# Performance work log

Hardware: AMD Instinct MI355X
Metric: run time of the kernel (lower is better)

## Reference

```python
import jax, jax.numpy as jnp
import numpy as np

NEG_INF = -1e30  # finite stand-in for -inf (fp16/bf16-safe)


def _ctc_loss(log_probs, labels):
    """CTC negative log-likelihood per example (blank index = 0).

    log_probs: [T, B, V] log-softmaxed logits (time-major, as tf.nn.ctc_loss default)
    labels:    [B, L] int labels in [1, V)
    returns:   [B] per-example loss
    """
    T, B, V = log_probs.shape
    L = labels.shape[1]
    S = 2 * L + 1  # blank-interleaved extended label length
    ext = jnp.zeros((B, S), labels.dtype).at[:, 1::2].set(labels)  # b_l1_b_l2_..._b
    # skip transition (s-2 -> s) allowed iff ext[s] != blank and ext[s] != ext[s-2]
    skip = jnp.concatenate(
        [jnp.zeros((B, 2), bool),
         (ext[:, 2:] != 0) & (ext[:, 2:] != ext[:, :-2])], axis=1)  # [B, S]

    def emit(lp_t):  # gather emission log-probs at extended label ids: [B,V]->[B,S]
        return jnp.take_along_axis(lp_t, ext, axis=1)

    # alpha[0]: only first blank and first label are reachable
    alpha0 = jnp.where(jnp.arange(S) < 2, emit(log_probs[0]), NEG_INF)  # [B, S]

    def step(alpha, lp_t):
        a1 = jnp.pad(alpha[:, :-1], ((0, 0), (1, 0)), constant_values=NEG_INF)
        a2 = jnp.pad(alpha[:, :-2], ((0, 0), (2, 0)), constant_values=NEG_INF)
        a2 = jnp.where(skip, a2, NEG_INF)
        m = jnp.maximum(jnp.maximum(alpha, a1), a2)  # stable 3-way logsumexp
        comb = m + jnp.log(jnp.exp(alpha - m) + jnp.exp(a1 - m) + jnp.exp(a2 - m))
        return comb + emit(lp_t), None

    alphaT, _ = jax.lax.scan(step, alpha0, log_probs[1:])
    # valid terminal states: last blank or last label
    return -jnp.logaddexp(alphaT[:, -1], alphaT[:, -2])  # [B]


def setup_inputs() -> dict:
    key = jax.random.key(0)
    k1, k2 = jax.random.split(key)
    T, B, V, L = 512, 1024, 96, 48
    y_pred = jax.random.normal(k1, (T, B, V), dtype=jnp.float32)  # time-major logits
    y_true = jax.random.randint(k2, (B, L), 1, V, dtype=jnp.int32)  # avoid blank=0
    return {"y_true": y_true, "y_pred": y_pred}


def reference(y_true, y_pred):
    log_probs = jax.nn.log_softmax(y_pred, axis=-1)
    return jnp.mean(_ctc_loss(log_probs, y_true))
```

## Files before the change

### kernel.cpp

```cpp
#include <hip/hip_runtime.h>

#define TT 512
#define BB 1024
#define VV 96
#define LL 48

__device__ __forceinline__ int f2i(float x) { return __float_as_int(x); }
__device__ __forceinline__ float i2f(int x) { return __int_as_float(x); }

template <int CTRL, int RM, int BM, bool BC>
__device__ __forceinline__ float dppf(float old, float src) {
    return i2f(__builtin_amdgcn_update_dpp(f2i(old), f2i(src), CTRL, RM, BM, BC));
}

__device__ __forceinline__ float wave_sum(float v) {
    v += dppf<0xB1, 0xF, 0xF, true>(0.f, v);
    v += dppf<0x4E, 0xF, 0xF, true>(0.f, v);
    v += dppf<0x141, 0xF, 0xF, true>(0.f, v);
    v += dppf<0x140, 0xF, 0xF, true>(0.f, v);
    v += dppf<0x142, 0xA, 0xF, false>(0.f, v);
    v += dppf<0x143, 0xC, 0xF, false>(0.f, v);
    return i2f(__builtin_amdgcn_readlane(f2i(v), 63));
}

__device__ __forceinline__ float wave_max(float v) {
    v = fmaxf(v, dppf<0xB1, 0xF, 0xF, true>(0.f, v));
    v = fmaxf(v, dppf<0x4E, 0xF, 0xF, true>(0.f, v));
    v = fmaxf(v, dppf<0x141, 0xF, 0xF, true>(0.f, v));
    v = fmaxf(v, dppf<0x140, 0xF, 0xF, true>(0.f, v));
    v = fmaxf(v, dppf<0x142, 0xA, 0xF, false>(0.f, v));
    v = fmaxf(v, dppf<0x143, 0xC, 0xF, false>(0.f, v));
    return i2f(__builtin_amdgcn_readlane(f2i(v), 63));
}

__global__ __launch_bounds__(128) void ctc_split_packed(
        const int* __restrict__ labels,
        const float* __restrict__ yp,
        float* __restrict__ loss) {
    const int b = blockIdx.x;
    const int tid = threadIdx.x;
    const int wid = tid >> 6;
    const int l = tid & 63;
    const int* lb = labels + b * LL;

    const int ll = (l < 48) ? l : 47;
    const int lbl = lb[ll];
    const bool lab = (l < 48);
    const bool skF = (l >= 1) && lab && (lb[l - 1] != lbl);
    const bool skB = (l < 47) && (lb[l + 1] != lbl);

    const float* base = yp + (size_t)b * VV;
    const size_t rstep = (size_t)BB * VV;

    float2 ringD[8];
    float  ringL[8];
    float Ae, Ao;
    int S2 = 0;
    float Eb, El;

#define LOADROW(ROW, SLOT) { \
        const float* rp_ = base + (size_t)(ROW) * rstep; \
        ringD[SLOT] = *(const float2*)(rp_ + 2 * ll); \
        ringL[SLOT] = rp_[lbl]; }

#define STAGEA(SLOT) { \
        float ex0 = __expf(ringD[SLOT].x), ex1 = __expf(ringD[SLOT].y); \
        float exl = __expf(ringL[SLOT]); \
        float se = lab ? (ex0 + ex1) : 0.f; \
        float tot = wave_sum(se); \
        float r96 = 96.0f * __builtin_amdgcn_rcpf(tot); \
        Eb = i2f(__builtin_amdgcn_readfirstlane(f2i(ex0))) * r96; \
        El = lab ? exl * r96 : 0.f; }

#define RENORM { \
        float vm = fmaxf(Ae, Ao); \
        float m = wave_max(vm); \
        int eb_ = (f2i(m) >> 23) & 0xFF; \
        float sc = i2f((254 - eb_) << 23); \
        Ae *= sc; Ao *= sc; \
        S2 += eb_ - 127; }

    __shared__ float sBe[64];
    __shared__ float sBo[64];
    __shared__ int sS2b;

    if (wid == 0) {
        #pragma unroll
        for (int j = 0; j < 8; ++j) LOADROW(j, j)
        Ae = (l == 0) ? 1.f : 0.f;
        Ao = 0.f;
        STAGEA(0)
        LOADROW(8, 0)
        for (int o = 0; o < 8; ++o) {
            for (int u = 0; u < 4; ++u) {
                #pragma unroll
                for (int tt = 0; tt < 8; ++tt) {
                    const int k = 32 * o + 8 * u + tt;
                    float sh = dppf<0x138, 0xF, 0xF, false>(0.f, Ao);
                    float AeN = (Ae + sh) * Eb;
                    float AoN = (Ao + Ae + (skF ? sh : 0.f)) * El;
                    Ae = AeN; Ao = AoN;
                    STAGEA((tt + 1) & 7)
                    int kr = k + 9; if (kr > 255) kr = 255;
                    LOADROW(kr, (tt + 1) & 7)
                }
            }
            RENORM
        }
    } else {
        #pragma unroll
        for (int j = 0; j < 8; ++j) LOADROW(511 - j, j)
        Ae = (l == 48) ? 1.f : 0.f;
        Ao = (l == 47) ? 1.f : 0.f;
        STAGEA(0)
        LOADROW(511 - 8, 0)
        for (int o = 0; o < 8; ++o) {
            for (int u = 0; u < 4; ++u) {
                #pragma unroll
                for (int tt = 0; tt < 8; ++tt) {
                    const int k = 32 * o + 8 * u + tt;
                    float wE = Ae * Eb;
                    float wO = Ao * El;
                    float sE = dppf<0x130, 0xF, 0xF, false>(0.f, wE);
                    float sO = dppf<0x130, 0xF, 0xF, false>(0.f, wO);
                    Ae = wE + wO;
                    Ao = wO + sE + (skB ? sO : 0.f);
                    STAGEA((tt + 1) & 7)
                    int kr = k + 9; if (kr > 255) kr = 255;
                    LOADROW(511 - kr, (tt + 1) & 7)
                }
            }
            RENORM
        }
        sBe[l] = Ae;
        sBo[l] = Ao;
        if (l == 0) sS2b = S2;
    }
    __syncthreads();
    if (wid == 0) {
        double pd = (double)Ae * (double)sBe[l] + (double)Ao * (double)sBo[l];
        #pragma unroll
        for (int m = 1; m < 64; m <<= 1) pd += __shfl_xor(pd, m);
        if (l == 0) {
            long long ud = __double_as_longlong(pd);
            int eb = (int)((ud >> 52) & 0x7FF);
            double md = __longlong_as_double(
                (ud & 0x000FFFFFFFFFFFFFLL) | 0x3FF0000000000000LL);
            int s2tot = S2 + sS2b + (eb - 1023);
            loss[b] = 2336.946274031532f
                    - (float)s2tot * 0.6931471805599453f
                    - __logf((float)md);
        }
    }
#undef LOADROW
#undef STAGEA
#undef RENORM
}

__global__ __launch_bounds__(256) void ctc_mean_kernel(
        const float* __restrict__ loss, float* __restrict__ out) {
    const int tid = threadIdx.x;
    float v = loss[tid] + loss[tid + 256] + loss[tid + 512] + loss[tid + 768];
    #pragma unroll
    for (int m = 1; m < 64; m <<= 1) v += __shfl_xor(v, m);
    __shared__ float part[4];
    if ((tid & 63) == 0) part[tid >> 6] = v;
    __syncthreads();
    if (tid == 0) out[0] = (part[0] + part[1] + part[2] + part[3]) * (1.0f / (float)BB);
}

extern "C" void kernel_launch(void* const* d_in, const int* in_sizes, int n_in,
                              void* d_out, int out_size, void* d_ws, size_t ws_size,
                              hipStream_t stream) {
    const int* y_true = (const int*)d_in[0];
    const float* y_pred = (const float*)d_in[1];
    float* out = (float*)d_out;
    float* lossbuf = (float*)d_ws;

    ctc_split_packed<<<BB, 128, 0, stream>>>(y_true, y_pred, lossbuf);
    ctc_mean_kernel<<<1, 256, 0, stream>>>(lossbuf, out);
}
```

Baseline: 285.2 us.

## Precompute normalized emissions into LDS before running the CTC recurrence

The kernel now runs in two phases. First, each wave streams its 256 time rows, computes the softmax-normalized blank and label emissions, and stores them in shared memory, with label emissions stored as fp16. Then the forward and backward recurrences read these values from LDS through a 4-deep register prefetch. This takes the global loads, exps and wave reductions off the serial dependency chain of the recurrence. In exchange each block uses about 50 KB of LDS, which can lower blocks per CU, and the fp16 rounding of emissions adds error that compounds over the time steps.

```diff
diff --git a/kernel.cpp b/kernel.cpp
--- a/kernel.cpp
+++ b/kernel.cpp
@@ -1,4 +1,5 @@
 #include <hip/hip_runtime.h>
+#include <hip/hip_fp16.h>
 
 #define TT 512
 #define BB 1024
@@ -33,7 +34,7 @@
     return i2f(__builtin_amdgcn_readlane(f2i(v), 63));
 }
 
-__global__ __launch_bounds__(128) void ctc_split_packed(
+__global__ __launch_bounds__(128) void ctc_split_lds(
         const int* __restrict__ labels,
         const float* __restrict__ yp,
         float* __restrict__ loss) {
@@ -52,25 +53,49 @@
     const float* base = yp + (size_t)b * VV;
     const size_t rstep = (size_t)BB * VV;
 
-    float2 ringD[8];
-    float  ringL[8];
+    __shared__ __half sEl[2][256][48];
+    __shared__ float  sEb[2][256];
+    __shared__ float  sBe[64];
+    __shared__ float  sBo[64];
+    __shared__ int    sS2b;
+
+    {
+        float2 ringD[8];
+        float  ringL[8];
+        #pragma unroll
+        for (int j = 0; j < 8; ++j) {
+            const int row = wid ? (511 - j) : j;
+            const float* rp = base + (size_t)row * rstep;
+            ringD[j] = *(const float2*)(rp + 2 * ll);
+            ringL[j] = rp[lbl];
+        }
+        for (int o = 0; o < 32; ++o) {
+            #pragma unroll
+            for (int tt = 0; tt < 8; ++tt) {
+                const int j = 8 * o + tt;
+                float ex0 = __expf(ringD[tt].x), ex1 = __expf(ringD[tt].y);
+                float exl = __expf(ringL[tt]);
+                float se = lab ? (ex0 + ex1) : 0.f;
+                float tot = wave_sum(se);
+                float r96 = 96.0f * __builtin_amdgcn_rcpf(tot);
+                if (lab) sEl[wid][j][l] = __float2half(exl * r96);
+                if (l == 0) sEb[wid][j] = ex0 * r96;
+                int jn = j + 8; if (jn > 255) jn = 255;
+                const int row = wid ? (511 - jn) : jn;
+                const float* rp = base + (size_t)row * rstep;
+                ringD[tt] = *(const float2*)(rp + 2 * ll);
+                ringL[tt] = rp[lbl];
+            }
+        }
+    }
+
     float Ae, Ao;
     int S2 = 0;
-    float Eb, El;
-
-#define LOADROW(ROW, SLOT) { \
-        const float* rp_ = base + (size_t)(ROW) * rstep; \
-        ringD[SLOT] = *(const float2*)(rp_ + 2 * ll); \
-        ringL[SLOT] = rp_[lbl]; }
-
-#define STAGEA(SLOT) { \
-        float ex0 = __expf(ringD[SLOT].x), ex1 = __expf(ringD[SLOT].y); \
-        float exl = __expf(ringL[SLOT]); \
-        float se = lab ? (ex0 + ex1) : 0.f; \
-        float tot = wave_sum(se); \
-        float r96 = 96.0f * __builtin_amdgcn_rcpf(tot); \
-        Eb = i2f(__builtin_amdgcn_readfirstlane(f2i(ex0))) * r96; \
-        El = lab ? exl * r96 : 0.f; }
+    float EB0, EL0, EB1, EL1, EB2, EL2, EB3, EL3;
+
+#define LOADE(K, EB, EL) { \
+        EB = sEb[wid][K]; \
+        EL = lab ? __half2float(sEl[wid][K][ll]) : 0.f; }
 
 #define RENORM { \
         float vm = fmaxf(Ae, Ao); \
@@ -80,55 +105,60 @@
         Ae *= sc; Ao *= sc; \
         S2 += eb_ - 127; }
 
-    __shared__ float sBe[64];
-    __shared__ float sBo[64];
-    __shared__ int sS2b;
+#define FSTEP(K, EB, EL) { \
+        float sh = dppf<0x138, 0xF, 0xF, false>(0.f, Ao); \
+        float AeN = (Ae + sh) * EB; \
+        float AoN = (Ao + Ae + (skF ? sh : 0.f)) * EL; \
+        Ae = AeN; Ao = AoN; \
+        int kn = (K) + 4; if (kn > 255) kn = 255; \
+        LOADE(kn, EB, EL) }
+
+#define BSTEP(K, EB, EL) { \
+        float wE = Ae * EB; \
+        float wO = Ao * EL; \
+        float sE = dppf<0x130, 0xF, 0xF, false>(0.f, wE); \
+        float sO = dppf<0x130, 0xF, 0xF, false>(0.f, wO); \
+        Ae = wE + wO; \
+        Ao = wO + sE + (skB ? sO : 0.f); \
+        int kn = (K) + 4; if (kn > 255) kn = 255; \
+        LOADE(kn, EB, EL) }
+
+    LOADE(0, EB0, EL0)
+    LOADE(1, EB1, EL1)
+    LOADE(2, EB2, EL2)
+    LOADE(3, EB3, EL3)
 
     if (wid == 0) {
-        #pragma unroll
-        for (int j = 0; j < 8; ++j) LOADROW(j, j)
         Ae = (l == 0) ? 1.f : 0.f;
         Ao = 0.f;
-        STAGEA(0)
-        LOADROW(8, 0)
         for (int o = 0; o < 8; ++o) {
             for (int u = 0; u < 4; ++u) {
-                #pragma unroll
-                for (int tt = 0; tt < 8; ++tt) {
-                    const int k = 32 * o + 8 * u + tt;
-                    float sh = dppf<0x138, 0xF, 0xF, false>(0.f, Ao);
-                    float AeN = (Ae + sh) * Eb;
-                    float AoN = (Ao + Ae + (skF ? sh : 0.f)) * El;
-                    Ae = AeN; Ao = AoN;
-                    STAGEA((tt + 1) & 7)
-                    int kr = k + 9; if (kr > 255) kr = 255;
-                    LOADROW(kr, (tt + 1) & 7)
-                }
+                const int k0 = 32 * o + 8 * u;
+                FSTEP(k0 + 0, EB0, EL0)
+                FSTEP(k0 + 1, EB1, EL1)
+                FSTEP(k0 + 2, EB2, EL2)
+                FSTEP(k0 + 3, EB3, EL3)
+                FSTEP(k0 + 4, EB0, EL0)
+                FSTEP(k0 + 5, EB1, EL1)
+                FSTEP(k0 + 6, EB2, EL2)
+                FSTEP(k0 + 7, EB3, EL3)
             }
             RENORM
         }
     } else {
-        #pragma unroll
-        for (int j = 0; j < 8; ++j) LOADROW(511 - j, j)
         Ae = (l == 48) ? 1.f : 0.f;
         Ao = (l == 47) ? 1.f : 0.f;
-        STAGEA(0)
-        LOADROW(511 - 8, 0)
         for (int o = 0; o < 8; ++o) {
             for (int u = 0; u < 4; ++u) {
-                #pragma unroll
-                for (int tt = 0; tt < 8; ++tt) {
-                    const int k = 32 * o + 8 * u + tt;
-                    float wE = Ae * Eb;
-                    float wO = Ao * El;
-                    float sE = dppf<0x130, 0xF, 0xF, false>(0.f, wE);
-                    float sO = dppf<0x130, 0xF, 0xF, false>(0.f, wO);
-                    Ae = wE + wO;
-                    Ao = wO + sE + (skB ? sO : 0.f);
-                    STAGEA((tt + 1) & 7)
-                    int kr = k + 9; if (kr > 255) kr = 255;
-                    LOADROW(511 - kr, (tt + 1) & 7)
-                }
+                const int k0 = 32 * o + 8 * u;
+                BSTEP(k0 + 0, EB0, EL0)
+                BSTEP(k0 + 1, EB1, EL1)
+                BSTEP(k0 + 2, EB2, EL2)
+                BSTEP(k0 + 3, EB3, EL3)
+                BSTEP(k0 + 4, EB0, EL0)
+                BSTEP(k0 + 5, EB1, EL1)
+                BSTEP(k0 + 6, EB2, EL2)
+                BSTEP(k0 + 7, EB3, EL3)
             }
             RENORM
         }
@@ -152,9 +182,10 @@
                     - __logf((float)md);
         }
     }
-#undef LOADROW
-#undef STAGEA
+#undef LOADE
 #undef RENORM
+#undef FSTEP
+#undef BSTEP
 }
 
 __global__ __launch_bounds__(256) void ctc_mean_kernel(
@@ -177,6 +208,6 @@
     float* out = (float*)d_out;
     float* lossbuf = (float*)d_ws;
 
-    ctc_split_packed<<<BB, 128, 0, stream>>>(y_true, y_pred, lossbuf);
+    ctc_split_lds<<<BB, 128, 0, stream>>>(y_true, y_pred, lossbuf);
     ctc_mean_kernel<<<1, 256, 0, stream>>>(lossbuf, out);
 }
```

Measured after the change: 326.3 us. +14.4%, slower.

## Stage coalesced time rows for eight batches in LDS and split directions into blocks

Applied to the files above, without the earlier changes.

Each 512-thread block now handles eight consecutive batch elements in one direction. The waves cooperatively load contiguous float4 slices of each time row (eight batches × 96 vocab) into shared memory, prefetching two chunks ahead, and each wave then reads its own emissions from LDS. The forward and backward passes run in separate blocks, and a new combine kernel joins the half-results through workspace. The goal is coalesced, wide global loads in place of per-lane scattered gathers. The cost is two __syncthreads per 8-step chunk, an extra kernel launch, and a workspace round trip.

```diff
diff --git a/kernel.cpp b/kernel.cpp
--- a/kernel.cpp
+++ b/kernel.cpp
@@ -4,6 +4,7 @@
 #define BB 1024
 #define VV 96
 #define LL 48
+#define NCH 32
 
 __device__ __forceinline__ int f2i(float x) { return __float_as_int(x); }
 __device__ __forceinline__ float i2f(int x) { return __int_as_float(x); }
@@ -33,128 +34,128 @@
     return i2f(__builtin_amdgcn_readlane(f2i(v), 63));
 }
 
-__global__ __launch_bounds__(128) void ctc_split_packed(
+__global__ __launch_bounds__(512) void ctc_halves(
         const int* __restrict__ labels,
         const float* __restrict__ yp,
-        float* __restrict__ loss) {
-    const int b = blockIdx.x;
+        float* __restrict__ ws) {
+    const int bgrp = blockIdx.x & 127;
+    const int dir  = blockIdx.x >> 7;
     const int tid = threadIdx.x;
-    const int wid = tid >> 6;
+    const int w = tid >> 6;
     const int l = tid & 63;
+    const int b = bgrp * 8 + w;
     const int* lb = labels + b * LL;
 
-    const int ll = (l < 48) ? l : 47;
+    const int ll  = (l < 48) ? l : 47;
     const int lbl = lb[ll];
     const bool lab = (l < 48);
     const bool skF = (l >= 1) && lab && (lb[l - 1] != lbl);
     const bool skB = (l < 47) && (lb[l + 1] != lbl);
 
-    const float* base = yp + (size_t)b * VV;
     const size_t rstep = (size_t)BB * VV;
+    const float* gbase = yp + (size_t)bgrp * (8 * VV);
 
-    float2 ringD[8];
-    float  ringL[8];
+    __shared__ float sE[8 * 768];
+
+    auto rowp = [&](int c) -> const float4* {
+        const int k = 8 * c + w;
+        const int t = dir ? (511 - k) : k;
+        return (const float4*)(gbase + (size_t)t * rstep);
+    };
+
+    float4 p0, p1, p2, q0, q1, q2;
+
+    { const float4* rp = rowp(0); p0 = rp[l]; p1 = rp[64 + l]; p2 = rp[128 + l]; }
+    { float4* dst = (float4*)&sE[w * 768]; dst[l] = p0; dst[64 + l] = p1; dst[128 + l] = p2; }
+    { const float4* rp = rowp(1); p0 = rp[l]; p1 = rp[64 + l]; p2 = rp[128 + l]; }
+    q0 = p0; q1 = p1; q2 = p2;
+    __syncthreads();
+
     float Ae, Ao;
     int S2 = 0;
-    float Eb, El;
+    if (dir == 0) { Ae = (l == 0) ? 1.f : 0.f; Ao = 0.f; }
+    else          { Ae = (l == 48) ? 1.f : 0.f; Ao = (l == 47) ? 1.f : 0.f; }
 
-#define LOADROW(ROW, SLOT) { \
-        const float* rp_ = base + (size_t)(ROW) * rstep; \
-        ringD[SLOT] = *(const float2*)(rp_ + 2 * ll); \
-        ringL[SLOT] = rp_[lbl]; }
+    for (int c = 0; c < NCH; ++c) {
+        float Ebv[8], Elv[8];
+        #pragma unroll
+        for (int r = 0; r < 8; ++r) {
+            const float* rb = &sE[r * 768 + w * 96];
+            float2 d = *(const float2*)(rb + 2 * ll);
+            float elg = rb[lbl];
+            float ex0 = __expf(d.x), ex1 = __expf(d.y), exl = __expf(elg);
+            float se = lab ? (ex0 + ex1) : 0.f;
+            float tot = wave_sum(se);
+            float r96 = 96.0f * __builtin_amdgcn_rcpf(tot);
+            Ebv[r] = i2f(__builtin_amdgcn_readfirstlane(f2i(ex0))) * r96;
+            Elv[r] = lab ? exl * r96 : 0.f;
+        }
+        if (c + 2 < NCH) {
+            const float4* rp = rowp(c + 2);
+            q0 = rp[l]; q1 = rp[64 + l]; q2 = rp[128 + l];
+        }
+        if (dir == 0) {
+            #pragma unroll
+            for (int r = 0; r < 8; ++r) {
+                float sh = dppf<0x138, 0xF, 0xF, false>(0.f, Ao);
+                float AeN = (Ae + sh) * Ebv[r];
+                float AoN = (Ao + Ae + (skF ? sh : 0.f)) * Elv[r];
+                Ae = AeN; Ao = AoN;
+            }
+        } else {
+            #pragma unroll
+            for (int r = 0; r < 8; ++r) {
+                float wE = Ae * Ebv[r];
+                float wO = Ao * Elv[r];
+                float shE = dppf<0x130, 0xF, 0xF, false>(0.f, wE);
+                float shO = dppf<0x130, 0xF, 0xF, false>(0.f, wO);
+                Ae = wE + wO;
+                Ao = wO + shE + (skB ? shO : 0.f);
+            }
+        }
+        if ((c & 3) == 3) {
+            float vm = fmaxf(Ae, Ao);
+            float m = wave_max(vm);
+            int eb_ = (f2i(m) >> 23) & 0xFF;
+            float sc = i2f((254 - eb_) << 23);
+            Ae *= sc; Ao *= sc;
+            S2 += eb_ - 127;
+        }
+        __syncthreads();
+        if (c + 1 < NCH) {
+            float4* dst = (float4*)&sE[w * 768];
+            dst[l] = p0; dst[64 + l] = p1; dst[128 + l] = p2;
+        }
+        p0 = q0; p1 = q1; p2 = q2;
+        __syncthreads();
+    }
 
-#define STAGEA(SLOT) { \
-        float ex0 = __expf(ringD[SLOT].x), ex1 = __expf(ringD[SLOT].y); \
-        float exl = __expf(ringL[SLOT]); \
-        float se = lab ? (ex0 + ex1) : 0.f; \
-        float tot = wave_sum(se); \
-        float r96 = 96.0f * __builtin_amdgcn_rcpf(tot); \
-        Eb = i2f(__builtin_amdgcn_readfirstlane(f2i(ex0))) * r96; \
-        El = lab ? exl * r96 : 0.f; }
+    float* out = ws + ((size_t)b * 2 + dir) * 132;
+    out[l] = Ae;
+    out[64 + l] = Ao;
+    if (l == 0) ((int*)out)[128] = S2;
+}
 
-#define RENORM { \
-        float vm = fmaxf(Ae, Ao); \
-        float m = wave_max(vm); \
-        int eb_ = (f2i(m) >> 23) & 0xFF; \
-        float sc = i2f((254 - eb_) << 23); \
-        Ae *= sc; Ao *= sc; \
-        S2 += eb_ - 127; }
-
-    __shared__ float sBe[64];
-    __shared__ float sBo[64];
-    __shared__ int sS2b;
-
-    if (wid == 0) {
-        #pragma unroll
-        for (int j = 0; j < 8; ++j) LOADROW(j, j)
-        Ae = (l == 0) ? 1.f : 0.f;
-        Ao = 0.f;
-        STAGEA(0)
-        LOADROW(8, 0)
-        for (int o = 0; o < 8; ++o) {
-            for (int u = 0; u < 4; ++u) {
-                #pragma unroll
-                for (int tt = 0; tt < 8; ++tt) {
-                    const int k = 32 * o + 8 * u + tt;
-                    float sh = dppf<0x138, 0xF, 0xF, false>(0.f, Ao);
-                    float AeN = (Ae + sh) * Eb;
-                    float AoN = (Ao + Ae + (skF ? sh : 0.f)) * El;
-                    Ae = AeN; Ao = AoN;
-                    STAGEA((tt + 1) & 7)
-                    int kr = k + 9; if (kr > 255) kr = 255;
-                    LOADROW(kr, (tt + 1) & 7)
-                }
-            }
-            RENORM
-        }
-    } else {
-        #pragma unroll
-        for (int j = 0; j < 8; ++j) LOADROW(511 - j, j)
-        Ae = (l == 48) ? 1.f : 0.f;
-        Ao = (l == 47) ? 1.f : 0.f;
-        STAGEA(0)
-        LOADROW(511 - 8, 0)
-        for (int o = 0; o < 8; ++o) {
-            for (int u = 0; u < 4; ++u) {
-                #pragma unroll
-                for (int tt = 0; tt < 8; ++tt) {
-                    const int k = 32 * o + 8 * u + tt;
-                    float wE = Ae * Eb;
-                    float wO = Ao * El;
-                    float sE = dppf<0x130, 0xF, 0xF, false>(0.f, wE);
-                    float sO = dppf<0x130, 0xF, 0xF, false>(0.f, wO);
-                    Ae = wE + wO;
-                    Ao = wO + sE + (skB ? sO : 0.f);
-                    STAGEA((tt + 1) & 7)
-                    int kr = k + 9; if (kr > 255) kr = 255;
-                    LOADROW(511 - kr, (tt + 1) & 7)
-                }
-            }
-            RENORM
-        }
-        sBe[l] = Ae;
-        sBo[l] = Ao;
-        if (l == 0) sS2b = S2;
+__global__ __launch_bounds__(256) void ctc_combine(
+        const float* __restrict__ ws, float* __restrict__ loss) {
+    const int b = blockIdx.x * 4 + (threadIdx.x >> 6);
+    const int l = threadIdx.x & 63;
+    const float* fb = ws + (size_t)(2 * b) * 132;
+    const float* bw = ws + (size_t)(2 * b + 1) * 132;
+    double pd = (double)fb[l] * bw[l] + (double)fb[64 + l] * bw[64 + l];
+    #pragma unroll
+    for (int m = 1; m < 64; m <<= 1) pd += __shfl_xor(pd, m);
+    if (l == 0) {
+        int s2 = ((const int*)fb)[128] + ((const int*)bw)[128];
+        long long ud = __double_as_longlong(pd);
+        int eb = (int)((ud >> 52) & 0x7FF);
+        double md = __longlong_as_double(
+            (ud & 0x000FFFFFFFFFFFFFLL) | 0x3FF0000000000000LL);
+        int s2tot = s2 + (eb - 1023);
+        loss[b] = 2336.946274031532f
+                - (float)s2tot * 0.6931471805599453f
+                - __logf((float)md);
     }
-    __syncthreads();
-    if (wid == 0) {
-        double pd = (double)Ae * (double)sBe[l] + (double)Ao * (double)sBo[l];
-        #pragma unroll
-        for (int m = 1; m < 64; m <<= 1) pd += __shfl_xor(pd, m);
-        if (l == 0) {
-            long long ud = __double_as_longlong(pd);
-            int eb = (int)((ud >> 52) & 0x7FF);
-            double md = __longlong_as_double(
-                (ud & 0x000FFFFFFFFFFFFFLL) | 0x3FF0000000000000LL);
-            int s2tot = S2 + sS2b + (eb - 1023);
-            loss[b] = 2336.946274031532f
-                    - (float)s2tot * 0.6931471805599453f
-                    - __logf((float)md);
-        }
-    }
-#undef LOADROW
-#undef STAGEA
-#undef RENORM
 }
 
 __global__ __launch_bounds__(256) void ctc_mean_kernel(
@@ -175,8 +176,11 @@
     const int* y_true = (const int*)d_in[0];
     const float* y_pred = (const float*)d_in[1];
     float* out = (float*)d_out;
-    float* lossbuf = (float*)d_ws;
 
-    ctc_split_packed<<<BB, 128, 0, stream>>>(y_true, y_pred, lossbuf);
+    float* ws = (float*)d_ws;
+    float* lossbuf = ws + (size_t)BB * 2 * 132;
+
+    ctc_halves<<<256, 512, 0, stream>>>(y_true, y_pred, ws);
+    ctc_combine<<<256, 256, 0, stream>>>(ws, lossbuf);
     ctc_mean_kernel<<<1, 256, 0, stream>>>(lossbuf, out);
 }
```

Result: faster. 276.4 us (-3.1%).
